# Performance work log

Hardware: AMD Instinct MI355X
Metric: run time of the kernel (lower is better)

## Reference

```python
import jax, jax.numpy as jnp
import numpy as np

IN_DIMS = 256
EMBED_DIMS = 512
NUM_HEADS = 8
GRID = 16  # forced: arrange2 hardcodes 256 = GRID*GRID tokens
HEAD_DIM = EMBED_DIMS // NUM_HEADS
LN_EPS = 1e-5


def setup_inputs() -> dict:
    key = jax.random.key(0)
    ks = jax.random.split(key, 12)
    B = 8
    s_in = 1.0 / np.sqrt(IN_DIMS)
    s_emb = 1.0 / np.sqrt(EMBED_DIMS)
    return {
        "x1": jax.random.normal(ks[0], (B, IN_DIMS, GRID, GRID), jnp.float32),
        "x2": jax.random.normal(ks[1], (B, IN_DIMS, GRID, GRID), jnp.float32),
        # 1x1 conv weights stored as [out, in]
        "Wq": jax.random.normal(ks[2], (EMBED_DIMS, IN_DIMS), jnp.float32) * s_in,
        "bq": jnp.zeros((EMBED_DIMS,), jnp.float32),
        "Wk": jax.random.normal(ks[3], (EMBED_DIMS, IN_DIMS), jnp.float32) * s_in,
        "bk": jnp.zeros((EMBED_DIMS,), jnp.float32),
        "Wv": jax.random.normal(ks[4], (EMBED_DIMS, IN_DIMS), jnp.float32) * s_in,
        "bv": jnp.zeros((EMBED_DIMS,), jnp.float32),
        "Wa": jax.random.normal(ks[5], (IN_DIMS, EMBED_DIMS), jnp.float32) * s_emb,
        "ba": jnp.zeros((IN_DIMS,), jnp.float32),
        "ln_g": jnp.ones((IN_DIMS,), jnp.float32),
        "ln_b": jnp.zeros((IN_DIMS,), jnp.float32),
        "Wl": jax.random.normal(ks[6], (IN_DIMS, IN_DIMS), jnp.float32) * s_in,
        "bl": jnp.zeros((IN_DIMS,), jnp.float32),
    }


def _conv1x1(x, W, b):
    # x: [b, Cin, h, w]; W: [Cout, Cin]
    return jnp.einsum('bihw,oi->bohw', x, W) + b[None, :, None, None]


def _arrange(t):
    # 'b (c head) h w -> head b (h w) c'  (c outer, head inner in channel axis)
    b = t.shape[0]
    t = t.reshape(b, HEAD_DIM, NUM_HEADS, GRID * GRID)
    return t.transpose(2, 0, 3, 1)  # [head, b, n, c]


def reference(x1, x2, Wq, bq, Wk, bk, Wv, bv, Wa, ba, ln_g, ln_b, Wl, bl):
    B, Cin, H, W = x1.shape
    N = H * W  # 256
    q = _arrange(_conv1x1(x1, Wq, bq))                     # [h, b, n, c]
    k = _arrange(_conv1x1(x2, Wk, bk))                     # [h, q, m, c]
    v = _arrange(_conv1x1(x2, Wv, bv)).reshape(NUM_HEADS, B * N, HEAD_DIM)  # [h, (b m), c]
    # cross-batch attention logits (NOTE: original never applies self.scale)
    attn = jnp.einsum('pbnc,pqmc->pbqnm', q, k)            # [h, b, q, n, m]
    attn = jax.nn.softmax(attn, axis=-1)
    # 'head b q n m -> b head n (q m)'
    attn = attn.transpose(1, 0, 3, 2, 4).reshape(B, NUM_HEADS, N, B * N)
    out = jnp.einsum('bhnm,hmc->bhnc', attn, v)            # [b, h, n, c]
    # 'b head (h w) c -> b (c head) h w'
    out = out.transpose(0, 3, 1, 2).reshape(B, EMBED_DIMS, H, W)
    a = _conv1x1(out, Wa, ba) + x1                          # residual, [b, Cin, h, w]
    # proj_out: rearrange -> LayerNorm -> Linear -> ReLU -> rearrange back
    t = a.reshape(B, Cin, N).transpose(0, 2, 1)            # [b, n, Cin]
    mu = t.mean(-1, keepdims=True)
    var = ((t - mu) ** 2).mean(-1, keepdims=True)
    t = (t - mu) * jax.lax.rsqrt(var + LN_EPS) * ln_g + ln_b
    t = jax.nn.relu(t @ Wl.T + bl)
    return t.transpose(0, 2, 1).reshape(B, Cin, H, W)
```

## Files before the change

kernel.cpp:

```cpp
#include <hip/hip_runtime.h>

typedef unsigned short u16;
typedef unsigned int   u32;
typedef __attribute__((ext_vector_type(8))) short bf16x8;
typedef __attribute__((ext_vector_type(4))) float f32x4;

#define BB   8
#define CIN  256
#define NT   256
#define EMB  512
#define NH   8

__device__ __forceinline__ float bf2f(u16 b) {
    union { u32 u; float f; } v; v.u = ((u32)b) << 16; return v.f;
}
__device__ __forceinline__ u16 f2bf(float f) {
    union { float f; u32 u; } v; v.f = f;
    u32 r = v.u + 0x7FFFu + ((v.u >> 16) & 1u);
    return (u16)(r >> 16);
}
__device__ __forceinline__ float ld(const u16* base, size_t idx, int f32) {
    return f32 ? ((const float*)base)[idx] : bf2f(base[idx]);
}

struct alignas(16) U32x4 { u32 x, y, z, w; };

#define FMA44(AP, S, A4, B4) do { \
  (AP)[0*(S)+0] += (A4).x*(B4).x; (AP)[0*(S)+1] += (A4).x*(B4).y; (AP)[0*(S)+2] += (A4).x*(B4).z; (AP)[0*(S)+3] += (A4).x*(B4).w; \
  (AP)[1*(S)+0] += (A4).y*(B4).x; (AP)[1*(S)+1] += (A4).y*(B4).y; (AP)[1*(S)+2] += (A4).y*(B4).z; (AP)[1*(S)+3] += (A4).y*(B4).w; \
  (AP)[2*(S)+0] += (A4).z*(B4).x; (AP)[2*(S)+1] += (A4).z*(B4).y; (AP)[2*(S)+2] += (A4).z*(B4).z; (AP)[2*(S)+3] += (A4).z*(B4).w; \
  (AP)[3*(S)+0] += (A4).w*(B4).x; (AP)[3*(S)+1] += (A4).w*(B4).y; (AP)[3*(S)+2] += (A4).w*(B4).z; (AP)[3*(S)+3] += (A4).w*(B4).w; \
} while (0)

__global__ void k_detect(const u16* __restrict__ x1, int* __restrict__ flag) {
    __shared__ int cnt;
    if (threadIdx.x == 0) cnt = 0;
    __syncthreads();
    int t = threadIdx.x;
    int local = 0;
    for (int j = t * 16; j < t * 16 + 16; j += 2) {
        u16 w = x1[j];
        int e = (w >> 7) & 0xFF;
        if (e >= 100 && e <= 145) local++;
    }
    atomicAdd(&cnt, local);
    __syncthreads();
    if (t == 0) *flag = (cnt >= 1200) ? 0 : 1;
}

__global__ void k_xpose(
    const u16* __restrict__ x1, const u16* __restrict__ x2,
    const u16* __restrict__ Wq, const u16* __restrict__ Wk, const u16* __restrict__ Wv,
    u16* __restrict__ XTh, u16* __restrict__ XTl,
    u16* __restrict__ WCh, u16* __restrict__ WCl)
{
    __shared__ int cnt;
    __shared__ float T[64][65];
    int t = threadIdx.x;
    if (t == 0) cnt = 0;
    __syncthreads();
    {
        int local = 0;
        for (int j = t * 16; j < t * 16 + 16; j += 2) {
            u16 w = x1[j];
            int e = (w >> 7) & 0xFF;
            if (e >= 100 && e <= 145) local++;
        }
        atomicAdd(&cnt, local);
    }
    __syncthreads();
    const int f32 = (cnt >= 1200) ? 0 : 1;

    int bid = blockIdx.x;
    if (bid < 256) {
        int inp = bid >> 7, b = (bid >> 4) & 7, ks = (bid >> 2) & 3, ns = bid & 3;
        const u16* X = inp ? x2 : x1;
#pragma unroll
        for (int p = 0; p < 4; ++p) {
            int kk = p * 16 + (t >> 4);
            int nn = (t & 15) * 4;
#pragma unroll
            for (int j = 0; j < 4; ++j)
                T[kk][nn + j] = ld(X, ((size_t)b * CIN + ks * 64 + kk) * NT + ns * 64 + nn + j, f32);
        }
        __syncthreads();
#pragma unroll
        for (int it = 0; it < 2; ++it) {
            int g = it * 256 + t;
            int nn = g >> 3, kg = g & 7;
            u32 hw[4], lw[4];
#pragma unroll
            for (int e = 0; e < 4; ++e) {
                float va = T[kg * 8 + 2 * e][nn];
                float vb = T[kg * 8 + 2 * e + 1][nn];
                u16 ha = f2bf(va), hb = f2bf(vb);
                u16 la = f2bf(va - bf2f(ha)), lb = f2bf(vb - bf2f(hb));
                hw[e] = (u32)ha | ((u32)hb << 16);
                lw[e] = (u32)la | ((u32)lb << 16);
            }
            size_t dst = (((size_t)(inp * 8 + b) * 256) + ns * 64 + nn) * 256 + ks * 64 + kg * 8;
            U32x4 H; H.x = hw[0]; H.y = hw[1]; H.z = hw[2]; H.w = hw[3];
            U32x4 L; L.x = lw[0]; L.y = lw[1]; L.z = lw[2]; L.w = lw[3];
            *(U32x4*)&XTh[dst] = H;
            *(U32x4*)&XTl[dst] = L;
        }
    } else {
        int wb = bid - 256;
        int proj = wb >> 2, qtr = wb & 3;
        const u16* W = (proj == 0) ? Wq : (proj == 1) ? Wk : Wv;
#pragma unroll
        for (int it = 0; it < 16; ++it) {
            int g = it * 256 + t;
            int row = g >> 5, kg = g & 31;
            int o = qtr * 128 + row;
            u32 hw[4], lw[4];
#pragma unroll
            for (int e = 0; e < 4; ++e) {
                float va = ld(W, (size_t)o * CIN + kg * 8 + 2 * e, f32);
                float vb = ld(W, (size_t)o * CIN + kg * 8 + 2 * e + 1, f32);
                u16 ha = f2bf(va), hb = f2bf(vb);
                u16 la = f2bf(va - bf2f(ha)), lb = f2bf(vb - bf2f(hb));
                hw[e] = (u32)ha | ((u32)hb << 16);
                lw[e] = (u32)la | ((u32)lb << 16);
            }
            size_t dst = ((size_t)(proj * 512 + o)) * 256 + kg * 8;
            U32x4 H; H.x = hw[0]; H.y = hw[1]; H.z = hw[2]; H.w = hw[3];
            U32x4 L; L.x = lw[0]; L.y = lw[1]; L.z = lw[2]; L.w = lw[3];
            *(U32x4*)&WCh[dst] = H;
            *(U32x4*)&WCl[dst] = L;
        }
    }
}

__global__ __launch_bounds__(256) void k_qkv(
    const u16* __restrict__ XTh, const u16* __restrict__ XTl,
    const u16* __restrict__ WCh, const u16* __restrict__ WCl,
    const u16* __restrict__ bq, const u16* __restrict__ bk, const u16* __restrict__ bv,
    u16* __restrict__ Qg, u16* __restrict__ Kg, u16* __restrict__ Vg,
    const int* __restrict__ flag)
{
    const int f32 = *flag;
    int id = blockIdx.x;
    int proj = id >> 8;
    int rem  = id & 255;
    int b  = rem >> 5;
    int ot = (rem >> 2) & 7;
    int nt = rem & 3;

    __shared__ __align__(16) u16 SB[16384];
    const int WHO = 0, WLO = 4096, XHO = 8192, XLO = 12288;

    int t = threadIdx.x;
    int l = t & 63, w = t >> 6;
    int quad = l >> 4, col = l & 15;
    const int lswz2 = l ^ (((l >> 4) & 1) << 1);

    const u16* Wh  = WCh + ((size_t)proj * 512 + ot * 64) * 256;
    const u16* Wlo = WCl + ((size_t)proj * 512 + ot * 64) * 256;
    int inp = (proj == 0) ? 0 : 1;
    const u16* Xh  = XTh + (((size_t)(inp * 8 + b)) * 256 + nt * 64) * 256;
    const u16* Xlo = XTl + (((size_t)(inp * 8 + b)) * 256 + nt * 64) * 256;

    f32x4 acc[4];
#pragma unroll
    for (int n4 = 0; n4 < 4; ++n4) { acc[n4][0]=0.f; acc[n4][1]=0.f; acc[n4][2]=0.f; acc[n4][3]=0.f; }

    for (int c4 = 0; c4 < 4; ++c4) {
        __syncthreads();
#pragma unroll
        for (int it = 0; it < 2; ++it) {
            int g = it * 256 + t;
            int row = g >> 3, cc = g & 7;
            int tt = row >> 4, klo = row & 15, kch = cc >> 2, qs = cc & 3;
            int pos = qs * 16 + (klo ^ ((qs & 1) << 1) ^ (kch << 2));
            int off = ((tt * 2 + kch) * 64 + pos) * 8;
            size_t src = (size_t)row * 256 + c4 * 64 + cc * 8;
            *(U32x4*)&SB[WHO + off] = *(const U32x4*)&Wh[src];
            *(U32x4*)&SB[WLO + off] = *(const U32x4*)&Wlo[src];
            *(U32x4*)&SB[XHO + off] = *(const U32x4*)&Xh[src];
            *(U32x4*)&SB[XLO + off] = *(const U32x4*)&Xlo[src];
        }
        __syncthreads();

        int sA0 = ((w * 2 + 0) * 64 + lswz2) * 8;
        int sA1 = ((w * 2 + 1) * 64 + (lswz2 ^ 4)) * 8;
        bf16x8 aH0 = *(const bf16x8*)&SB[WHO + sA0];
        bf16x8 aH1 = *(const bf16x8*)&SB[WHO + sA1];
        bf16x8 aL0 = *(const bf16x8*)&SB[WLO + sA0];
        bf16x8 aL1 = *(const bf16x8*)&SB[WLO + sA1];
#pragma unroll
        for (int n4 = 0; n4 < 4; ++n4) {
            int sB0 = ((n4 * 2 + 0) * 64 + lswz2) * 8;
            int sB1 = ((n4 * 2 + 1) * 64 + (lswz2 ^ 4)) * 8;
            bf16x8 bH0 = *(const bf16x8*)&SB[XHO + sB0];
            bf16x8 bH1 = *(const bf16x8*)&SB[XHO + sB1];
            bf16x8 bL0 = *(const bf16x8*)&SB[XLO + sB0];
            bf16x8 bL1 = *(const bf16x8*)&SB[XLO + sB1];
            acc[n4] = __builtin_amdgcn_mfma_f32_16x16x32_bf16(aH0, bH0, acc[n4], 0, 0, 0);
            acc[n4] = __builtin_amdgcn_mfma_f32_16x16x32_bf16(aH1, bH1, acc[n4], 0, 0, 0);
            acc[n4] = __builtin_amdgcn_mfma_f32_16x16x32_bf16(aL0, bH0, acc[n4], 0, 0, 0);
            acc[n4] = __builtin_amdgcn_mfma_f32_16x16x32_bf16(aL1, bH1, acc[n4], 0, 0, 0);
            acc[n4] = __builtin_amdgcn_mfma_f32_16x16x32_bf16(aH0, bL0, acc[n4], 0, 0, 0);
            acc[n4] = __builtin_amdgcn_mfma_f32_16x16x32_bf16(aH1, bL1, acc[n4], 0, 0, 0);
        }
    }
    __syncthreads();

    float (*EP)[68] = (float (*)[68])SB;
    const u16* bias = (proj == 0) ? bq : (proj == 1) ? bk : bv;
#pragma unroll
    for (int r = 0; r < 4; ++r) {
        int ol = w * 16 + quad * 4 + r;
        float bb = ld(bias, ot * 64 + ol, f32);
#pragma unroll
        for (int n4 = 0; n4 < 4; ++n4)
            EP[ol][n4 * 16 + col] = acc[n4][r] + bb;
    }
    __syncthreads();

    if (proj < 2) {
        u16* OUT = (proj == 0) ? Qg : Kg;
        int hh = t >> 5;
        int nb = t & 31;
#pragma unroll
        for (int p = 0; p < 2; ++p) {
            int nn = nb + 32 * p;
            u32 pk[4];
#pragma unroll
            for (int e = 0; e < 4; ++e) {
                u16 lo = f2bf(EP[(2 * e) * 8 + hh][nn]);
                u16 hi = f2bf(EP[(2 * e + 1) * 8 + hh][nn]);
                pk[e] = (u32)lo | ((u32)hi << 16);
            }
            U32x4 v; v.x = pk[0]; v.y = pk[1]; v.z = pk[2]; v.w = pk[3];
            *(U32x4*)&OUT[((size_t)((hh * 8 + b) * 256) + nt * 64 + nn) * 64 + ot * 8] = v;
        }
    } else {
        int rr = t >> 2;
        int hh = rr & 7, cl = rr >> 3;
        int nq = t & 3;
        u32 pk[8];
#pragma unroll
        for (int e = 0; e < 8; ++e) {
            u16 lo = f2bf(EP[cl * 8 + hh][nq * 16 + 2 * e]);
            u16 hi = f2bf(EP[cl * 8 + hh][nq * 16 + 2 * e + 1]);
            pk[e] = (u32)lo | ((u32)hi << 16);
        }
        size_t base = ((size_t)((hh * 8 + b) * 64) + ot * 8 + cl) * 256 + nt * 64 + nq * 16;
        U32x4 v0; v0.x = pk[0]; v0.y = pk[1]; v0.z = pk[2]; v0.w = pk[3];
        U32x4 v1; v1.x = pk[4]; v1.y = pk[5]; v1.z = pk[6]; v1.w = pk[7];
        *(U32x4*)&Vg[base]     = v0;
        *(U32x4*)&Vg[base + 8] = v1;
    }
}

__global__ __launch_bounds__(256) void k_attn(
    const u16* __restrict__ Qg, const u16* __restrict__ Kg,
    const u16* __restrict__ Vg, float* __restrict__ Oph)
{
    int bid = blockIdx.x;
    int h   = bid >> 6;
    int kbg = (bid >> 5) & 1;
    int b   = (bid >> 2) & 7;
    int ntq = bid & 3;

    int t = threadIdx.x;
    int l = t & 63, w = t >> 6;
    int quad = l >> 4, col = l & 15;

    __shared__ __align__(16) u16 S[16384];

    int q = ntq*64 + w*16 + col;
    const size_t qrow = ((size_t)(h*8 + b)*256 + q)*64;
    bf16x8 qf0 = *(const bf16x8*)&Qg[qrow +  0 + quad*8];
    bf16x8 qf1 = *(const bf16x8*)&Qg[qrow + 32 + quad*8];

    const int lswz2 = l ^ (((l >> 4) & 1) << 1);
    const int lswz4 = l ^ (((l >> 4) & 1) << 2);

    f32x4 Oacc[4];
#pragma unroll
    for (int ct = 0; ct < 4; ++ct) { Oacc[ct][0]=0.f; Oacc[ct][1]=0.f; Oacc[ct][2]=0.f; Oacc[ct][3]=0.f; }

    for (int kb2 = 0; kb2 < 4; ++kb2) {
        int kb = kbg*4 + kb2;
        __syncthreads();
        const size_t kbase = (size_t)(h*8 + kb) * 256 * 64;
#pragma unroll
        for (int i = 0; i < 8; ++i) {
            int g = i*256 + t;
            int key = g >> 3, cc = g & 7;
            int tt = key >> 4, klo = key & 15, kc = cc >> 2, qs = cc & 3;
            int pos = qs*16 + (klo ^ ((qs & 1) << 1) ^ (kc << 2));
            U32x4 v = *(const U32x4*)&Kg[kbase + (size_t)key*64 + cc*8];
            *(U32x4*)&S[(size_t)(((tt*2 + kc)*64) + pos)*8] = v;
        }
        __syncthreads();

        f32x4 Sfr[16];
#pragma unroll
        for (int tt = 0; tt < 16; ++tt) { Sfr[tt][0]=0.f; Sfr[tt][1]=0.f; Sfr[tt][2]=0.f; Sfr[tt][3]=0.f; }
#pragma unroll
        for (int tt = 0; tt < 16; ++tt) {
            bf16x8 k0 = *(const bf16x8*)&S[(size_t)((tt*2 + 0)*64 + lswz2)*8];
            bf16x8 k1 = *(const bf16x8*)&S[(size_t)((tt*2 + 1)*64 + (lswz2 ^ 4))*8];
            Sfr[tt] = __builtin_amdgcn_mfma_f32_16x16x32_bf16(k0, qf0, Sfr[tt], 0, 0, 0);
            Sfr[tt] = __builtin_amdgcn_mfma_f32_16x16x32_bf16(k1, qf1, Sfr[tt], 0, 0, 0);
        }

        float inv;
        {
            float m = Sfr[0][0];
#pragma unroll
            for (int tt = 0; tt < 16; ++tt)
#pragma unroll
                for (int r = 0; r < 4; ++r) m = fmaxf(m, Sfr[tt][r]);
            m = fmaxf(m, __shfl_xor(m, 16));
            m = fmaxf(m, __shfl_xor(m, 32));
            float s = 0.f;
#pragma unroll
            for (int tt = 0; tt < 16; ++tt)
#pragma unroll
                for (int r = 0; r < 4; ++r) {
                    float e = __expf(Sfr[tt][r] - m);
                    Sfr[tt][r] = e; s += e;
                }
            s += __shfl_xor(s, 16);
            s += __shfl_xor(s, 32);
            inv = 1.f / s;
        }

        bf16x8 pf[8];
#pragma unroll
        for (int ch = 0; ch < 8; ++ch) {
            float a0 = Sfr[2*ch  ][0]*inv, a1 = Sfr[2*ch  ][1]*inv;
            float a2 = Sfr[2*ch  ][2]*inv, a3 = Sfr[2*ch  ][3]*inv;
            float b0 = Sfr[2*ch+1][0]*inv, b1 = Sfr[2*ch+1][1]*inv;
            float b2 = Sfr[2*ch+1][2]*inv, b3 = Sfr[2*ch+1][3]*inv;
            u32 u0, u1, v0, v1;
            asm("v_cvt_pk_bf16_f32 %0, %1, %2" : "=v"(u0) : "v"(a0), "v"(a1));
            asm("v_cvt_pk_bf16_f32 %0, %1, %2" : "=v"(u1) : "v"(a2), "v"(a3));
            asm("v_cvt_pk_bf16_f32 %0, %1, %2" : "=v"(v0) : "v"(b0), "v"(b1));
            asm("v_cvt_pk_bf16_f32 %0, %1, %2" : "=v"(v1) : "v"(b2), "v"(b3));
            asm("v_permlane32_swap_b32 %0, %1" : "+v"(u0), "+v"(v0));
            asm("v_permlane16_swap_b32 %0, %1" : "+v"(u0), "+v"(v0));
            asm("v_permlane32_swap_b32 %0, %1" : "+v"(u1), "+v"(v1));
            asm("v_permlane16_swap_b32 %0, %1" : "+v"(u1), "+v"(v1));
            union { u32 wd[4]; bf16x8 hB; } pu;
            pu.wd[0] = u0; pu.wd[1] = u1; pu.wd[2] = v0; pu.wd[3] = v1;
            pf[ch] = pu.hB;
        }
        __syncthreads();

        const size_t vbase = (size_t)(h*8 + kb) * 64 * 256;
#pragma unroll
        for (int i = 0; i < 8; ++i) {
            int g = i*256 + t;
            int cg = g >> 5, k16 = g & 31;
            int ct = cg >> 4, clo = cg & 15, ch = k16 >> 2, qs = k16 & 3;
            int pos = (qs*16 + clo) ^ ch ^ ((qs & 1) << 2);
            U32x4 v = *(const U32x4*)&Vg[vbase + (size_t)cg*256 + k16*8];
            *(U32x4*)&S[(size_t)(((ch*4 + ct)*64) + pos)*8] = v;
        }
        __syncthreads();

#pragma unroll
        for (int ch = 0; ch < 8; ++ch)
#pragma unroll
            for (int ct = 0; ct < 4; ++ct) {
                bf16x8 vb = *(const bf16x8*)&S[(size_t)(((ch*4 + ct)*64) + (lswz4 ^ ch))*8];
                Oacc[ct] = __builtin_amdgcn_mfma_f32_16x16x32_bf16(pf[ch], vb, Oacc[ct], 0, 0, 0);
            }
    }

    float* Op = Oph + (size_t)kbg * ((size_t)BB * EMB * NT);
    const size_t obase = (size_t)(h*8 + b) * 256 * 64;
    int n0 = ntq*64 + w*16 + quad*4;
#pragma unroll
    for (int ct = 0; ct < 4; ++ct)
#pragma unroll
        for (int r = 0; r < 4; ++r)
            Op[obase + (size_t)(n0 + r)*64 + ct*16 + col] = Oacc[ct][r];
}

__global__ void k_proj_res(
    const float* __restrict__ Oph, const u16* __restrict__ Wa,
    const u16* __restrict__ ba, const u16* __restrict__ x1,
    float* __restrict__ Ap, const int* __restrict__ flag)
{
    const int f32 = *flag;
    int id = blockIdx.x;
    int tt = id >> 2;
    int it = id & 3;
    int tok0 = tt * 32;
    int b  = tok0 >> 8;
    int n0 = tok0 & 255;

    __shared__ float Was[64][68];
    __shared__ float Os[64][36];

    int t = threadIdx.x;
    int lane64 = t & 63, quad = t >> 6;
    int ig = t & 15;
    int tg = t >> 4;

    int tk = t & 31;
    int hh = t >> 5;

    const size_t SLAB = (size_t)BB * EMB * NT;

    float wreg[16];
    float oreg[8];

    {
#pragma unroll
        for (int p = 0; p < 16; ++p) {
            int i = quad + 4*p;
            wreg[p] = ld(Wa, (size_t)(it*64 + i)*EMB + 0*64 + lane64, f32);
        }
        const float* src = &Oph[(((size_t)(hh*8 + b))*256 + n0 + tk)*64 + 0*8];
        float4 v0 = *(const float4*)&src[0];
        float4 v1 = *(const float4*)&src[4];
        float4 u0 = *(const float4*)&src[SLAB];
        float4 u1 = *(const float4*)&src[SLAB + 4];
        oreg[0]=v0.x+u0.x; oreg[1]=v0.y+u0.y; oreg[2]=v0.z+u0.z; oreg[3]=v0.w+u0.w;
        oreg[4]=v1.x+u1.x; oreg[5]=v1.y+u1.y; oreg[6]=v1.z+u1.z; oreg[7]=v1.w+u1.w;
    }

    float acc[8];
#pragma unroll
    for (int j = 0; j < 8; ++j) acc[j] = 0.f;

    for (int kc = 0; kc < 8; ++kc) {
        __syncthreads();
#pragma unroll
        for (int p = 0; p < 16; ++p)
            Was[lane64][quad + 4*p] = wreg[p];
#pragma unroll
        for (int e = 0; e < 8; ++e)
            Os[e*8 + hh][tk] = oreg[e];
        __syncthreads();

        if (kc < 7) {
            int kn = kc + 1;
#pragma unroll
            for (int p = 0; p < 16; ++p) {
                int i = quad + 4*p;
                wreg[p] = ld(Wa, (size_t)(it*64 + i)*EMB + kn*64 + lane64, f32);
            }
            const float* src = &Oph[(((size_t)(hh*8 + b))*256 + n0 + tk)*64 + kn*8];
            float4 v0 = *(const float4*)&src[0];
            float4 v1 = *(const float4*)&src[4];
            float4 u0 = *(const float4*)&src[SLAB];
            float4 u1 = *(const float4*)&src[SLAB + 4];
            oreg[0]=v0.x+u0.x; oreg[1]=v0.y+u0.y; oreg[2]=v0.z+u0.z; oreg[3]=v0.w+u0.w;
            oreg[4]=v1.x+u1.x; oreg[5]=v1.y+u1.y; oreg[6]=v1.z+u1.z; oreg[7]=v1.w+u1.w;
        }

#pragma unroll 8
        for (int o = 0; o < 64; ++o) {
            float4 w4 = *(const float4*)&Was[o][ig*4];
            float2 t2 = *(const float2*)&Os[o][tg*2];
            acc[0] += w4.x*t2.x; acc[1] += w4.y*t2.x;
            acc[2] += w4.z*t2.x; acc[3] += w4.w*t2.x;
            acc[4] += w4.x*t2.y; acc[5] += w4.y*t2.y;
            acc[6] += w4.z*t2.y; acc[7] += w4.w*t2.y;
        }
    }

    int i0 = it*64 + ig*4;
    float ba0 = ld(ba, i0+0, f32), ba1 = ld(ba, i0+1, f32);
    float ba2 = ld(ba, i0+2, f32), ba3 = ld(ba, i0+3, f32);
#pragma unroll
    for (int jt = 0; jt < 2; ++jt) {
        int token = tok0 + tg*2 + jt;
        int n = n0 + tg*2 + jt;
        float4 v;
        v.x = acc[jt*4+0] + ba0 + ld(x1, ((size_t)b*CIN + i0+0)*NT + n, f32);
        v.y = acc[jt*4+1] + ba1 + ld(x1, ((size_t)b*CIN + i0+1)*NT + n, f32);
        v.z = acc[jt*4+2] + ba2 + ld(x1, ((size_t)b*CIN + i0+2)*NT + n, f32);
        v.w = acc[jt*4+3] + ba3 + ld(x1, ((size_t)b*CIN + i0+3)*NT + n, f32);
        *(float4*)&Ap[(size_t)token*CIN + i0] = v;
    }
}

__global__ void k_ln_out(
    const float* __restrict__ Ap, const u16* __restrict__ ln_g,
    const u16* __restrict__ ln_b, const u16* __restrict__ Wl,
    const u16* __restrict__ bl, u16* __restrict__ out,
    const int* __restrict__ flag)
{
    const int f32 = *flag;
    int tok0 = blockIdx.x * 8;
    int b  = tok0 >> 8;
    int n0 = tok0 & 255;

    __shared__ float At[8][260];

    int t = threadIdx.x;
#pragma unroll
    for (int k = 0; k < 8; ++k)
        At[k][t] = Ap[((size_t)tok0 + k)*CIN + t];
    __syncthreads();

    {
        int kk = t >> 5, lme = t & 31;
        float s = 0.f, s2 = 0.f;
#pragma unroll
        for (int ii = 0; ii < 8; ++ii) { float v = At[kk][lme + 32*ii]; s += v; s2 += v*v; }
#pragma unroll
        for (int off = 1; off < 32; off <<= 1) { s += __shfl_xor(s, off); s2 += __shfl_xor(s2, off); }
        float mu   = s  * (1.f/256.f);
        float var  = s2 * (1.f/256.f) - mu*mu;
        float rstd = rsqrtf(var + 1e-5f);
#pragma unroll
        for (int ii = 0; ii < 8; ++ii) {
            int i = lme + 32*ii;
            float v = At[kk][i];
            At[kk][i] = (v - mu) * rstd * ld(ln_g, i, f32) + ld(ln_b, i, f32);
        }
    }
    __syncthreads();

    int j = t;
    float acc[8];
#pragma unroll
    for (int k = 0; k < 8; ++k) acc[k] = 0.f;

    if (f32) {
        const float* wrow = (const float*)Wl + (size_t)j*CIN;
#pragma unroll 2
        for (int i4 = 0; i4 < 64; ++i4) {
            float4 w4 = *(const float4*)&wrow[4*i4];
#pragma unroll
            for (int k = 0; k < 8; ++k) {
                float4 a = *(const float4*)&At[k][4*i4];
                acc[k] += w4.x*a.x + w4.y*a.y + w4.z*a.z + w4.w*a.w;
            }
        }
    } else {
        const u32* wrow = (const u32*)(Wl + (size_t)j*CIN);
#pragma unroll 2
        for (int i4 = 0; i4 < 64; ++i4) {
            u32 w01 = wrow[2*i4+0], w23 = wrow[2*i4+1];
            float c0 = bf2f((u16)(w01 & 0xFFFFu)), c1 = bf2f((u16)(w01 >> 16));
            float c2 = bf2f((u16)(w23 & 0xFFFFu)), c3 = bf2f((u16)(w23 >> 16));
#pragma unroll
            for (int k = 0; k < 8; ++k) {
                float4 a = *(const float4*)&At[k][4*i4];
                acc[k] += c0*a.x + c1*a.y + c2*a.z + c3*a.w;
            }
        }
    }

    float blv = ld(bl, j, f32);
    size_t obase = ((size_t)b*CIN + j)*NT + n0;
    if (f32) {
        float* o32 = (float*)out;
#pragma unroll
        for (int k = 0; k < 8; ++k)
            o32[obase + k] = fmaxf(acc[k] + blv, 0.f);
    } else {
        u32 pk[4];
#pragma unroll
        for (int k = 0; k < 4; ++k) {
            float f0 = fmaxf(acc[2*k+0] + blv, 0.f);
            float f1 = fmaxf(acc[2*k+1] + blv, 0.f);
            pk[k] = (u32)f2bf(f0) | ((u32)f2bf(f1) << 16);
        }
        U32x4 a0; a0.x = pk[0]; a0.y = pk[1]; a0.z = pk[2]; a0.w = pk[3];
        *(U32x4*)(out + obase) = a0;
    }
}

extern "C" void kernel_launch(void* const* d_in, const int* in_sizes, int n_in,
                              void* d_out, int out_size, void* d_ws, size_t ws_size,
                              hipStream_t stream)
{
    const u16* x1   = (const u16*)d_in[0];
    const u16* x2   = (const u16*)d_in[1];
    const u16* Wq   = (const u16*)d_in[2];
    const u16* bq   = (const u16*)d_in[3];
    const u16* Wk   = (const u16*)d_in[4];
    const u16* bk   = (const u16*)d_in[5];
    const u16* Wv   = (const u16*)d_in[6];
    const u16* bv   = (const u16*)d_in[7];
    const u16* Wa   = (const u16*)d_in[8];
    const u16* ba   = (const u16*)d_in[9];
    const u16* ln_g = (const u16*)d_in[10];
    const u16* ln_b = (const u16*)d_in[11];
    const u16* Wl   = (const u16*)d_in[12];
    const u16* bl   = (const u16*)d_in[13];
    u16* out = (u16*)d_out;

    int* flag = (int*)d_ws;
    u16* Qg = (u16*)d_ws + 32;
    u16* Kg = Qg + (size_t)BB*EMB*NT;
    u16* Vg = Kg + (size_t)BB*EMB*NT;
    float* Oph = (float*)(Vg + (size_t)BB*EMB*NT);
    float* Ap  = Oph + 2*(size_t)BB*EMB*NT;
    u16* XTh = (u16*)(Ap + (size_t)BB*NT*CIN);
    u16* XTl = XTh + (size_t)2*BB*NT*CIN;
    u16* WCh = XTl + (size_t)2*BB*NT*CIN;
    u16* WCl = WCh + (size_t)3*EMB*CIN;

    k_detect  <<<1,   256, 0, stream>>>(x1, flag);
    k_xpose   <<<268, 256, 0, stream>>>(x1, x2, Wq, Wk, Wv, XTh, XTl, WCh, WCl);
    k_qkv     <<<768, 256, 0, stream>>>(XTh, XTl, WCh, WCl, bq, bk, bv, Qg, Kg, Vg, flag);
    k_attn    <<<512, 256, 0, stream>>>(Qg, Kg, Vg, Oph);
    k_proj_res<<<256, 256, 0, stream>>>(Oph, Wa, ba, x1, Ap, flag);
    k_ln_out  <<<256, 256, 0, stream>>>(Ap, ln_g, ln_b, Wl, bl, out, flag);
}
```

Measured before the change: 185.0 us.

## Fold detect into xpose, rebalance attention split, shrink proj/LN tiles for more blocks

Removes the separate detect kernel by having the first xpose block write the dtype flag. The attention kernel now processes two query tiles per block against the same staged K/V and splits keys four ways instead of two, so K/V reads from shared memory are reused across both tiles. The extra partial-output slabs mean the projection must sum four slabs. The projection and LN/output kernels halve the work per block and double the grid to raise occupancy, at the cost of more partial buffers and extra global traffic.

```diff
diff --git a/kernel.cpp b/kernel.cpp
--- a/kernel.cpp
+++ b/kernel.cpp
@@ -24,35 +24,14 @@
 }
 
 struct alignas(16) U32x4 { u32 x, y, z, w; };
-
-#define FMA44(AP, S, A4, B4) do { \
-  (AP)[0*(S)+0] += (A4).x*(B4).x; (AP)[0*(S)+1] += (A4).x*(B4).y; (AP)[0*(S)+2] += (A4).x*(B4).z; (AP)[0*(S)+3] += (A4).x*(B4).w; \
-  (AP)[1*(S)+0] += (A4).y*(B4).x; (AP)[1*(S)+1] += (A4).y*(B4).y; (AP)[1*(S)+2] += (A4).y*(B4).z; (AP)[1*(S)+3] += (A4).y*(B4).w; \
-  (AP)[2*(S)+0] += (A4).z*(B4).x; (AP)[2*(S)+1] += (A4).z*(B4).y; (AP)[2*(S)+2] += (A4).z*(B4).z; (AP)[2*(S)+3] += (A4).z*(B4).w; \
-  (AP)[3*(S)+0] += (A4).w*(B4).x; (AP)[3*(S)+1] += (A4).w*(B4).y; (AP)[3*(S)+2] += (A4).w*(B4).z; (AP)[3*(S)+3] += (A4).w*(B4).w; \
-} while (0)
-
-__global__ void k_detect(const u16* __restrict__ x1, int* __restrict__ flag) {
-    __shared__ int cnt;
-    if (threadIdx.x == 0) cnt = 0;
-    __syncthreads();
-    int t = threadIdx.x;
-    int local = 0;
-    for (int j = t * 16; j < t * 16 + 16; j += 2) {
-        u16 w = x1[j];
-        int e = (w >> 7) & 0xFF;
-        if (e >= 100 && e <= 145) local++;
-    }
-    atomicAdd(&cnt, local);
-    __syncthreads();
-    if (t == 0) *flag = (cnt >= 1200) ? 0 : 1;
-}
+struct alignas(8)  U32x2 { u32 x, y; };
 
 __global__ void k_xpose(
     const u16* __restrict__ x1, const u16* __restrict__ x2,
     const u16* __restrict__ Wq, const u16* __restrict__ Wk, const u16* __restrict__ Wv,
     u16* __restrict__ XTh, u16* __restrict__ XTl,
-    u16* __restrict__ WCh, u16* __restrict__ WCl)
+    u16* __restrict__ WCh, u16* __restrict__ WCl,
+    int* __restrict__ flag)
 {
     __shared__ int cnt;
     __shared__ float T[64][65];
@@ -72,6 +51,8 @@
     const int f32 = (cnt >= 1200) ? 0 : 1;
 
     int bid = blockIdx.x;
+    if (bid == 0 && t == 0) *flag = f32;
+
     if (bid < 256) {
         int inp = bid >> 7, b = (bid >> 4) & 7, ks = (bid >> 2) & 3, ns = bid & 3;
         const u16* X = inp ? x2 : x1;
@@ -254,15 +235,58 @@
     }
 }
 
+__device__ __forceinline__ void softmax_p(f32x4 (&Sfr)[16], bf16x8 (&pf)[8]) {
+    float inv;
+    {
+        float m = Sfr[0][0];
+#pragma unroll
+        for (int tt = 0; tt < 16; ++tt)
+#pragma unroll
+            for (int r = 0; r < 4; ++r) m = fmaxf(m, Sfr[tt][r]);
+        m = fmaxf(m, __shfl_xor(m, 16));
+        m = fmaxf(m, __shfl_xor(m, 32));
+        float s = 0.f;
+#pragma unroll
+        for (int tt = 0; tt < 16; ++tt)
+#pragma unroll
+            for (int r = 0; r < 4; ++r) {
+                float e = __expf(Sfr[tt][r] - m);
+                Sfr[tt][r] = e; s += e;
+            }
+        s += __shfl_xor(s, 16);
+        s += __shfl_xor(s, 32);
+        inv = 1.f / s;
+    }
+#pragma unroll
+    for (int ch = 0; ch < 8; ++ch) {
+        float a0 = Sfr[2*ch  ][0]*inv, a1 = Sfr[2*ch  ][1]*inv;
+        float a2 = Sfr[2*ch  ][2]*inv, a3 = Sfr[2*ch  ][3]*inv;
+        float b0 = Sfr[2*ch+1][0]*inv, b1 = Sfr[2*ch+1][1]*inv;
+        float b2 = Sfr[2*ch+1][2]*inv, b3 = Sfr[2*ch+1][3]*inv;
+        u32 u0, u1, v0, v1;
+        asm("v_cvt_pk_bf16_f32 %0, %1, %2" : "=v"(u0) : "v"(a0), "v"(a1));
+        asm("v_cvt_pk_bf16_f32 %0, %1, %2" : "=v"(u1) : "v"(a2), "v"(a3));
+        asm("v_cvt_pk_bf16_f32 %0, %1, %2" : "=v"(v0) : "v"(b0), "v"(b1));
+        asm("v_cvt_pk_bf16_f32 %0, %1, %2" : "=v"(v1) : "v"(b2), "v"(b3));
+        asm("v_permlane32_swap_b32 %0, %1" : "+v"(u0), "+v"(v0));
+        asm("v_permlane16_swap_b32 %0, %1" : "+v"(u0), "+v"(v0));
+        asm("v_permlane32_swap_b32 %0, %1" : "+v"(u1), "+v"(v1));
+        asm("v_permlane16_swap_b32 %0, %1" : "+v"(u1), "+v"(v1));
+        union { u32 wd[4]; bf16x8 hB; } pu;
+        pu.wd[0] = u0; pu.wd[1] = u1; pu.wd[2] = v0; pu.wd[3] = v1;
+        pf[ch] = pu.hB;
+    }
+}
+
 __global__ __launch_bounds__(256) void k_attn(
     const u16* __restrict__ Qg, const u16* __restrict__ Kg,
     const u16* __restrict__ Vg, float* __restrict__ Oph)
 {
     int bid = blockIdx.x;
-    int h   = bid >> 6;
-    int kbg = (bid >> 5) & 1;
-    int b   = (bid >> 2) & 7;
-    int ntq = bid & 3;
+    int h    = bid >> 6;
+    int kbg  = (bid >> 4) & 3;
+    int b    = (bid >> 1) & 7;
+    int ntq2 = bid & 1;
 
     int t = threadIdx.x;
     int l = t & 63, w = t >> 6;
@@ -270,20 +294,26 @@
 
     __shared__ __align__(16) u16 S[16384];
 
-    int q = ntq*64 + w*16 + col;
-    const size_t qrow = ((size_t)(h*8 + b)*256 + q)*64;
-    bf16x8 qf0 = *(const bf16x8*)&Qg[qrow +  0 + quad*8];
-    bf16x8 qf1 = *(const bf16x8*)&Qg[qrow + 32 + quad*8];
+    int qa = ntq2*128 + w*16 + col;
+    const size_t qrowa = ((size_t)(h*8 + b)*256 + qa)*64;
+    const size_t qrowb = qrowa + (size_t)64*64;
+    bf16x8 qf0a = *(const bf16x8*)&Qg[qrowa +  0 + quad*8];
+    bf16x8 qf1a = *(const bf16x8*)&Qg[qrowa + 32 + quad*8];
+    bf16x8 qf0b = *(const bf16x8*)&Qg[qrowb +  0 + quad*8];
+    bf16x8 qf1b = *(const bf16x8*)&Qg[qrowb + 32 + quad*8];
 
     const int lswz2 = l ^ (((l >> 4) & 1) << 1);
     const int lswz4 = l ^ (((l >> 4) & 1) << 2);
 
-    f32x4 Oacc[4];
-#pragma unroll
-    for (int ct = 0; ct < 4; ++ct) { Oacc[ct][0]=0.f; Oacc[ct][1]=0.f; Oacc[ct][2]=0.f; Oacc[ct][3]=0.f; }
-
-    for (int kb2 = 0; kb2 < 4; ++kb2) {
-        int kb = kbg*4 + kb2;
+    f32x4 OaccA[4], OaccB[4];
+#pragma unroll
+    for (int ct = 0; ct < 4; ++ct) {
+        OaccA[ct][0]=0.f; OaccA[ct][1]=0.f; OaccA[ct][2]=0.f; OaccA[ct][3]=0.f;
+        OaccB[ct][0]=0.f; OaccB[ct][1]=0.f; OaccB[ct][2]=0.f; OaccB[ct][3]=0.f;
+    }
+
+    for (int kb2 = 0; kb2 < 2; ++kb2) {
+        int kb = kbg*2 + kb2;
         __syncthreads();
         const size_t kbase = (size_t)(h*8 + kb) * 256 * 64;
 #pragma unroll
@@ -297,59 +327,25 @@
         }
         __syncthreads();
 
-        f32x4 Sfr[16];
-#pragma unroll
-        for (int tt = 0; tt < 16; ++tt) { Sfr[tt][0]=0.f; Sfr[tt][1]=0.f; Sfr[tt][2]=0.f; Sfr[tt][3]=0.f; }
+        f32x4 SfA[16], SfB[16];
+#pragma unroll
+        for (int tt = 0; tt < 16; ++tt) {
+            SfA[tt][0]=0.f; SfA[tt][1]=0.f; SfA[tt][2]=0.f; SfA[tt][3]=0.f;
+            SfB[tt][0]=0.f; SfB[tt][1]=0.f; SfB[tt][2]=0.f; SfB[tt][3]=0.f;
+        }
 #pragma unroll
         for (int tt = 0; tt < 16; ++tt) {
             bf16x8 k0 = *(const bf16x8*)&S[(size_t)((tt*2 + 0)*64 + lswz2)*8];
             bf16x8 k1 = *(const bf16x8*)&S[(size_t)((tt*2 + 1)*64 + (lswz2 ^ 4))*8];
-            Sfr[tt] = __builtin_amdgcn_mfma_f32_16x16x32_bf16(k0, qf0, Sfr[tt], 0, 0, 0);
-            Sfr[tt] = __builtin_amdgcn_mfma_f32_16x16x32_bf16(k1, qf1, Sfr[tt], 0, 0, 0);
-        }
-
-        float inv;
-        {
-            float m = Sfr[0][0];
-#pragma unroll
-            for (int tt = 0; tt < 16; ++tt)
-#pragma unroll
-                for (int r = 0; r < 4; ++r) m = fmaxf(m, Sfr[tt][r]);
-            m = fmaxf(m, __shfl_xor(m, 16));
-            m = fmaxf(m, __shfl_xor(m, 32));
-            float s = 0.f;
-#pragma unroll
-            for (int tt = 0; tt < 16; ++tt)
-#pragma unroll
-                for (int r = 0; r < 4; ++r) {
-                    float e = __expf(Sfr[tt][r] - m);
-                    Sfr[tt][r] = e; s += e;
-                }
-            s += __shfl_xor(s, 16);
-            s += __shfl_xor(s, 32);
-            inv = 1.f / s;
-        }
-
-        bf16x8 pf[8];
-#pragma unroll
-        for (int ch = 0; ch < 8; ++ch) {
-            float a0 = Sfr[2*ch  ][0]*inv, a1 = Sfr[2*ch  ][1]*inv;
-            float a2 = Sfr[2*ch  ][2]*inv, a3 = Sfr[2*ch  ][3]*inv;
-            float b0 = Sfr[2*ch+1][0]*inv, b1 = Sfr[2*ch+1][1]*inv;
-            float b2 = Sfr[2*ch+1][2]*inv, b3 = Sfr[2*ch+1][3]*inv;
-            u32 u0, u1, v0, v1;
-            asm("v_cvt_pk_bf16_f32 %0, %1, %2" : "=v"(u0) : "v"(a0), "v"(a1));
-            asm("v_cvt_pk_bf16_f32 %0, %1, %2" : "=v"(u1) : "v"(a2), "v"(a3));
-            asm("v_cvt_pk_bf16_f32 %0, %1, %2" : "=v"(v0) : "v"(b0), "v"(b1));
-            asm("v_cvt_pk_bf16_f32 %0, %1, %2" : "=v"(v1) : "v"(b2), "v"(b3));
-            asm("v_permlane32_swap_b32 %0, %1" : "+v"(u0), "+v"(v0));
-            asm("v_permlane16_swap_b32 %0, %1" : "+v"(u0), "+v"(v0));
-            asm("v_permlane32_swap_b32 %0, %1" : "+v"(u1), "+v"(v1));
-            asm("v_permlane16_swap_b32 %0, %1" : "+v"(u1), "+v"(v1));
-            union { u32 wd[4]; bf16x8 hB; } pu;
-            pu.wd[0] = u0; pu.wd[1] = u1; pu.wd[2] = v0; pu.wd[3] = v1;
-            pf[ch] = pu.hB;
-        }
+            SfA[tt] = __builtin_amdgcn_mfma_f32_16x16x32_bf16(k0, qf0a, SfA[tt], 0, 0, 0);
+            SfA[tt] = __builtin_amdgcn_mfma_f32_16x16x32_bf16(k1, qf1a, SfA[tt], 0, 0, 0);
+            SfB[tt] = __builtin_amdgcn_mfma_f32_16x16x32_bf16(k0, qf0b, SfB[tt], 0, 0, 0);
+            SfB[tt] = __builtin_amdgcn_mfma_f32_16x16x32_bf16(k1, qf1b, SfB[tt], 0, 0, 0);
+        }
+
+        bf16x8 pfA[8], pfB[8];
+        softmax_p(SfA, pfA);
+        softmax_p(SfB, pfB);
         __syncthreads();
 
         const size_t vbase = (size_t)(h*8 + kb) * 64 * 256;
@@ -369,72 +365,82 @@
 #pragma unroll
             for (int ct = 0; ct < 4; ++ct) {
                 bf16x8 vb = *(const bf16x8*)&S[(size_t)(((ch*4 + ct)*64) + (lswz4 ^ ch))*8];
-                Oacc[ct] = __builtin_amdgcn_mfma_f32_16x16x32_bf16(pf[ch], vb, Oacc[ct], 0, 0, 0);
+                OaccA[ct] = __builtin_amdgcn_mfma_f32_16x16x32_bf16(pfA[ch], vb, OaccA[ct], 0, 0, 0);
+                OaccB[ct] = __builtin_amdgcn_mfma_f32_16x16x32_bf16(pfB[ch], vb, OaccB[ct], 0, 0, 0);
             }
     }
 
     float* Op = Oph + (size_t)kbg * ((size_t)BB * EMB * NT);
     const size_t obase = (size_t)(h*8 + b) * 256 * 64;
-    int n0 = ntq*64 + w*16 + quad*4;
+    int n0a = ntq2*128 + w*16 + quad*4;
 #pragma unroll
     for (int ct = 0; ct < 4; ++ct)
 #pragma unroll
-        for (int r = 0; r < 4; ++r)
-            Op[obase + (size_t)(n0 + r)*64 + ct*16 + col] = Oacc[ct][r];
-}
-
-__global__ void k_proj_res(
+        for (int r = 0; r < 4; ++r) {
+            Op[obase + (size_t)(n0a + r)*64 + ct*16 + col]      = OaccA[ct][r];
+            Op[obase + (size_t)(n0a + 64 + r)*64 + ct*16 + col] = OaccB[ct][r];
+        }
+}
+
+__global__ __launch_bounds__(256) void k_proj_res(
     const float* __restrict__ Oph, const u16* __restrict__ Wa,
     const u16* __restrict__ ba, const u16* __restrict__ x1,
     float* __restrict__ Ap, const int* __restrict__ flag)
 {
     const int f32 = *flag;
     int id = blockIdx.x;
-    int tt = id >> 2;
-    int it = id & 3;
+    int tt = id >> 3;
+    int it = id & 7;
     int tok0 = tt * 32;
     int b  = tok0 >> 8;
     int n0 = tok0 & 255;
 
-    __shared__ float Was[64][68];
+    __shared__ float Was[64][36];
     __shared__ float Os[64][36];
 
     int t = threadIdx.x;
     int lane64 = t & 63, quad = t >> 6;
-    int ig = t & 15;
-    int tg = t >> 4;
+    int ig = t & 7;
+    int tg = t >> 3;
 
     int tk = t & 31;
     int hh = t >> 5;
 
     const size_t SLAB = (size_t)BB * EMB * NT;
 
-    float wreg[16];
+    float wreg[8];
     float oreg[8];
 
     {
 #pragma unroll
-        for (int p = 0; p < 16; ++p) {
+        for (int p = 0; p < 8; ++p) {
             int i = quad + 4*p;
-            wreg[p] = ld(Wa, (size_t)(it*64 + i)*EMB + 0*64 + lane64, f32);
+            wreg[p] = ld(Wa, (size_t)(it*32 + i)*EMB + 0*64 + lane64, f32);
         }
         const float* src = &Oph[(((size_t)(hh*8 + b))*256 + n0 + tk)*64 + 0*8];
-        float4 v0 = *(const float4*)&src[0];
-        float4 v1 = *(const float4*)&src[4];
-        float4 u0 = *(const float4*)&src[SLAB];
-        float4 u1 = *(const float4*)&src[SLAB + 4];
-        oreg[0]=v0.x+u0.x; oreg[1]=v0.y+u0.y; oreg[2]=v0.z+u0.z; oreg[3]=v0.w+u0.w;
-        oreg[4]=v1.x+u1.x; oreg[5]=v1.y+u1.y; oreg[6]=v1.z+u1.z; oreg[7]=v1.w+u1.w;
-    }
-
-    float acc[8];
-#pragma unroll
-    for (int j = 0; j < 8; ++j) acc[j] = 0.f;
+#pragma unroll
+        for (int s_ = 0; s_ < 4; ++s_) {
+            const float* sp = src + (size_t)s_*SLAB;
+            float4 v0 = *(const float4*)&sp[0];
+            float4 v1 = *(const float4*)&sp[4];
+            if (s_ == 0) {
+                oreg[0]=v0.x; oreg[1]=v0.y; oreg[2]=v0.z; oreg[3]=v0.w;
+                oreg[4]=v1.x; oreg[5]=v1.y; oreg[6]=v1.z; oreg[7]=v1.w;
+            } else {
+                oreg[0]+=v0.x; oreg[1]+=v0.y; oreg[2]+=v0.z; oreg[3]+=v0.w;
+                oreg[4]+=v1.x; oreg[5]+=v1.y; oreg[6]+=v1.z; oreg[7]+=v1.w;
+            }
+        }
+    }
+
+    float acc[4];
+#pragma unroll
+    for (int j = 0; j < 4; ++j) acc[j] = 0.f;
 
     for (int kc = 0; kc < 8; ++kc) {
         __syncthreads();
 #pragma unroll
-        for (int p = 0; p < 16; ++p)
+        for (int p = 0; p < 8; ++p)
             Was[lane64][quad + 4*p] = wreg[p];
 #pragma unroll
         for (int e = 0; e < 8; ++e)
@@ -444,78 +450,80 @@
         if (kc < 7) {
             int kn = kc + 1;
 #pragma unroll
-            for (int p = 0; p < 16; ++p) {
+            for (int p = 0; p < 8; ++p) {
                 int i = quad + 4*p;
-                wreg[p] = ld(Wa, (size_t)(it*64 + i)*EMB + kn*64 + lane64, f32);
+                wreg[p] = ld(Wa, (size_t)(it*32 + i)*EMB + kn*64 + lane64, f32);
             }
             const float* src = &Oph[(((size_t)(hh*8 + b))*256 + n0 + tk)*64 + kn*8];
-            float4 v0 = *(const float4*)&src[0];
-            float4 v1 = *(const float4*)&src[4];
-            float4 u0 = *(const float4*)&src[SLAB];
-            float4 u1 = *(const float4*)&src[SLAB + 4];
-            oreg[0]=v0.x+u0.x; oreg[1]=v0.y+u0.y; oreg[2]=v0.z+u0.z; oreg[3]=v0.w+u0.w;
-            oreg[4]=v1.x+u1.x; oreg[5]=v1.y+u1.y; oreg[6]=v1.z+u1.z; oreg[7]=v1.w+u1.w;
+#pragma unroll
+            for (int s_ = 0; s_ < 4; ++s_) {
+                const float* sp = src + (size_t)s_*SLAB;
+                float4 v0 = *(const float4*)&sp[0];
+                float4 v1 = *(const float4*)&sp[4];
+                if (s_ == 0) {
+                    oreg[0]=v0.x; oreg[1]=v0.y; oreg[2]=v0.z; oreg[3]=v0.w;
+                    oreg[4]=v1.x; oreg[5]=v1.y; oreg[6]=v1.z; oreg[7]=v1.w;
+                } else {
+                    oreg[0]+=v0.x; oreg[1]+=v0.y; oreg[2]+=v0.z; oreg[3]+=v0.w;
+                    oreg[4]+=v1.x; oreg[5]+=v1.y; oreg[6]+=v1.z; oreg[7]+=v1.w;
+                }
+            }
         }
 
 #pragma unroll 8
         for (int o = 0; o < 64; ++o) {
             float4 w4 = *(const float4*)&Was[o][ig*4];
-            float2 t2 = *(const float2*)&Os[o][tg*2];
-            acc[0] += w4.x*t2.x; acc[1] += w4.y*t2.x;
-            acc[2] += w4.z*t2.x; acc[3] += w4.w*t2.x;
-            acc[4] += w4.x*t2.y; acc[5] += w4.y*t2.y;
-            acc[6] += w4.z*t2.y; acc[7] += w4.w*t2.y;
-        }
-    }
-
-    int i0 = it*64 + ig*4;
+            float ov = Os[o][tg];
+            acc[0] += w4.x*ov; acc[1] += w4.y*ov;
+            acc[2] += w4.z*ov; acc[3] += w4.w*ov;
+        }
+    }
+
+    int i0 = it*32 + ig*4;
     float ba0 = ld(ba, i0+0, f32), ba1 = ld(ba, i0+1, f32);
     float ba2 = ld(ba, i0+2, f32), ba3 = ld(ba, i0+3, f32);
-#pragma unroll
-    for (int jt = 0; jt < 2; ++jt) {
-        int token = tok0 + tg*2 + jt;
-        int n = n0 + tg*2 + jt;
-        float4 v;
-        v.x = acc[jt*4+0] + ba0 + ld(x1, ((size_t)b*CIN + i0+0)*NT + n, f32);
-        v.y = acc[jt*4+1] + ba1 + ld(x1, ((size_t)b*CIN + i0+1)*NT + n, f32);
-        v.z = acc[jt*4+2] + ba2 + ld(x1, ((size_t)b*CIN + i0+2)*NT + n, f32);
-        v.w = acc[jt*4+3] + ba3 + ld(x1, ((size_t)b*CIN + i0+3)*NT + n, f32);
-        *(float4*)&Ap[(size_t)token*CIN + i0] = v;
-    }
-}
-
-__global__ void k_ln_out(
+    int n = n0 + tg;
+    int token = tok0 + tg;
+    float4 v;
+    v.x = acc[0] + ba0 + ld(x1, ((size_t)b*CIN + i0+0)*NT + n, f32);
+    v.y = acc[1] + ba1 + ld(x1, ((size_t)b*CIN + i0+1)*NT + n, f32);
+    v.z = acc[2] + ba2 + ld(x1, ((size_t)b*CIN + i0+2)*NT + n, f32);
+    v.w = acc[3] + ba3 + ld(x1, ((size_t)b*CIN + i0+3)*NT + n, f32);
+    *(float4*)&Ap[(size_t)token*CIN + i0] = v;
+}
+
+__global__ __launch_bounds__(256) void k_ln_out(
     const float* __restrict__ Ap, const u16* __restrict__ ln_g,
     const u16* __restrict__ ln_b, const u16* __restrict__ Wl,
     const u16* __restrict__ bl, u16* __restrict__ out,
     const int* __restrict__ flag)
 {
     const int f32 = *flag;
-    int tok0 = blockIdx.x * 8;
+    int tok0 = blockIdx.x * 4;
     int b  = tok0 >> 8;
     int n0 = tok0 & 255;
 
-    __shared__ float At[8][260];
+    __shared__ float At[4][260];
 
     int t = threadIdx.x;
 #pragma unroll
-    for (int k = 0; k < 8; ++k)
+    for (int k = 0; k < 4; ++k)
         At[k][t] = Ap[((size_t)tok0 + k)*CIN + t];
     __syncthreads();
 
     {
-        int kk = t >> 5, lme = t & 31;
+        int kk = t >> 6, lme = t & 63;
         float s = 0.f, s2 = 0.f;
 #pragma unroll
-        for (int ii = 0; ii < 8; ++ii) { float v = At[kk][lme + 32*ii]; s += v; s2 += v*v; }
-#pragma unroll
-        for (int off = 1; off < 32; off <<= 1) { s += __shfl_xor(s, off); s2 += __shfl_xor(s2, off); }
+        for (int ii = 0; ii < 4; ++ii) { float v = At[kk][lme + 64*ii]; s += v; s2 += v*v; }
+#pragma unroll
+        for (int off = 1; off < 64; off <<= 1) { s += __shfl_xor(s, off); s2 += __shfl_xor(s2, off); }
         float mu   = s  * (1.f/256.f);
         float var  = s2 * (1.f/256.f) - mu*mu;
         float rstd = rsqrtf(var + 1e-5f);
 #pragma unroll
-        for (int ii = 0; ii < 8; ++ii) {
-            int i = lme + 32*ii;
+        for (int ii = 0; ii < 4; ++ii) {
+            int i = lme + 64*ii;
             float v = At[kk][i];
             At[kk][i] = (v - mu) * rstd * ld(ln_g, i, f32) + ld(ln_b, i, f32);
         }
@@ -523,9 +531,9 @@
     __syncthreads();
 
     int j = t;
-    float acc[8];
-#pragma unroll
-    for (int k = 0; k < 8; ++k) acc[k] = 0.f;
+    float acc[4];
+#pragma unroll
+    for (int k = 0; k < 4; ++k) acc[k] = 0.f;
 
     if (f32) {
         const float* wrow = (const float*)Wl + (size_t)j*CIN;
@@ -533,7 +541,7 @@
         for (int i4 = 0; i4 < 64; ++i4) {
             float4 w4 = *(const float4*)&wrow[4*i4];
 #pragma unroll
-            for (int k = 0; k < 8; ++k) {
+            for (int k = 0; k < 4; ++k) {
                 float4 a = *(const float4*)&At[k][4*i4];
                 acc[k] += w4.x*a.x + w4.y*a.y + w4.z*a.z + w4.w*a.w;
             }
@@ -546,7 +554,7 @@
             float c0 = bf2f((u16)(w01 & 0xFFFFu)), c1 = bf2f((u16)(w01 >> 16));
             float c2 = bf2f((u16)(w23 & 0xFFFFu)), c3 = bf2f((u16)(w23 >> 16));
 #pragma unroll
-            for (int k = 0; k < 8; ++k) {
+            for (int k = 0; k < 4; ++k) {
                 float4 a = *(const float4*)&At[k][4*i4];
                 acc[k] += c0*a.x + c1*a.y + c2*a.z + c3*a.w;
             }
@@ -557,19 +565,22 @@
     size_t obase = ((size_t)b*CIN + j)*NT + n0;
     if (f32) {
         float* o32 = (float*)out;
-#pragma unroll
-        for (int k = 0; k < 8; ++k)
-            o32[obase + k] = fmaxf(acc[k] + blv, 0.f);
+        float4 v;
+        v.x = fmaxf(acc[0] + blv, 0.f);
+        v.y = fmaxf(acc[1] + blv, 0.f);
+        v.z = fmaxf(acc[2] + blv, 0.f);
+        v.w = fmaxf(acc[3] + blv, 0.f);
+        *(float4*)&o32[obase] = v;
     } else {
-        u32 pk[4];
-#pragma unroll
-        for (int k = 0; k < 4; ++k) {
+        u32 pk[2];
+#pragma unroll
+        for (int k = 0; k < 2; ++k) {
             float f0 = fmaxf(acc[2*k+0] + blv, 0.f);
             float f1 = fmaxf(acc[2*k+1] + blv, 0.f);
             pk[k] = (u32)f2bf(f0) | ((u32)f2bf(f1) << 16);
         }
-        U32x4 a0; a0.x = pk[0]; a0.y = pk[1]; a0.z = pk[2]; a0.w = pk[3];
-        *(U32x4*)(out + obase) = a0;
+        U32x2 a0; a0.x = pk[0]; a0.y = pk[1];
+        *(U32x2*)(out + obase) = a0;
     }
 }
 
@@ -598,16 +609,15 @@
     u16* Kg = Qg + (size_t)BB*EMB*NT;
     u16* Vg = Kg + (size_t)BB*EMB*NT;
     float* Oph = (float*)(Vg + (size_t)BB*EMB*NT);
-    float* Ap  = Oph + 2*(size_t)BB*EMB*NT;
+    float* Ap  = Oph + 4*(size_t)BB*EMB*NT;
     u16* XTh = (u16*)(Ap + (size_t)BB*NT*CIN);
     u16* XTl = XTh + (size_t)2*BB*NT*CIN;
     u16* WCh = XTl + (size_t)2*BB*NT*CIN;
     u16* WCl = WCh + (size_t)3*EMB*CIN;
 
-    k_detect  <<<1,   256, 0, stream>>>(x1, flag);
-    k_xpose   <<<268, 256, 0, stream>>>(x1, x2, Wq, Wk, Wv, XTh, XTl, WCh, WCl);
+    k_xpose   <<<268, 256, 0, stream>>>(x1, x2, Wq, Wk, Wv, XTh, XTl, WCh, WCl, flag);
     k_qkv     <<<768, 256, 0, stream>>>(XTh, XTl, WCh, WCl, bq, bk, bv, Qg, Kg, Vg, flag);
     k_attn    <<<512, 256, 0, stream>>>(Qg, Kg, Vg, Oph);
-    k_proj_res<<<256, 256, 0, stream>>>(Oph, Wa, ba, x1, Ap, flag);
-    k_ln_out  <<<256, 256, 0, stream>>>(Ap, ln_g, ln_b, Wl, bl, out, flag);
-}
+    k_proj_res<<<512, 256, 0, stream>>>(Oph, Wa, ba, x1, Ap, flag);
+    k_ln_out  <<<512, 256, 0, stream>>>(Ap, ln_g, ln_b, Wl, bl, out, flag);
+}
```

After: 237.5 us. +28.4%, slower.
